# Performance work log

Hardware: AMD Instinct MI355X
Metric: run time of the kernel (lower is better)

The kernel has to match this reference:

```python
import jax, jax.numpy as jnp
import numpy as np

STATE_DIM = 32
ACTION_DIM = 8
IN_DIM = STATE_DIM + ACTION_DIM      # 40
DIMS = STATE_DIM + 1                 # 33 output dimensions (next-state deltas + reward)
ENS = 10                             # ensemble size
HID = 128
BATCH = 4096
MIN_LOGVAR = -10.0
MAX_LOGVAR = 5.0


def setup_inputs() -> dict:
    key = jax.random.key(0)
    ks = jax.random.split(key, 7)
    # Kaiming-uniform-ish init like torch Linear: U(-1/sqrt(fan_in), 1/sqrt(fan_in))
    def lin_init(k, shape, fan_in):
        bound = 1.0 / np.sqrt(fan_in)
        return jax.random.uniform(k, shape, jnp.float32, -bound, bound)
    x = jax.random.normal(ks[0], (BATCH, IN_DIM), jnp.float32)
    W1 = lin_init(ks[1], (DIMS, ENS, HID, IN_DIM), IN_DIM)
    b1 = lin_init(ks[2], (DIMS, ENS, HID), IN_DIM)
    W2 = lin_init(ks[3], (DIMS, ENS, HID, HID), HID)
    b2 = lin_init(ks[4], (DIMS, ENS, HID), HID)
    W3 = lin_init(ks[5], (DIMS, ENS, 2, HID), HID)
    b3 = lin_init(ks[6], (DIMS, ENS, 2), HID)
    return {"x": x, "W1": W1, "b1": b1, "W2": W2, "b2": b2, "W3": W3, "b3": b3}


def reference(x, W1, b1, W2, b2, W3, b3):
    # Batched over (d, e): all 330 small MLPs share the same input x.
    # h1: [B, D, E, H]
    h1 = jax.nn.silu(jnp.einsum('bi,dehi->bdeh', x, W1) + b1)
    h2 = jax.nn.silu(jnp.einsum('bdeh,degh->bdeg', h1, W2) + b2)
    out = jnp.einsum('bdeh,deoh->bdeo', h2, W3) + b3  # [B, D, E, 2]
    mean = out[..., 0]                                # [B, D, E]
    logvar = out[..., 1]
    # logvar soft clamp (same as original: two softplus bounds)
    logvar = MAX_LOGVAR - jax.nn.softplus(MAX_LOGVAR - logvar)
    logvar = MIN_LOGVAR + jax.nn.softplus(logvar - MIN_LOGVAR)
    # means[b, d, e] == means_all[d][e][b, 0] of the torch module
    return mean, logvar
```

## Files before the change

### kernel.cpp

```cpp
#include <hip/hip_runtime.h>

typedef _Float16 half8_t __attribute__((ext_vector_type(8)));
typedef float    f32x4_t __attribute__((ext_vector_type(4)));
typedef unsigned int uint4_t __attribute__((ext_vector_type(4)));

#define OUT_HALF 1351680
#define NDE 330

#define OFF_X16    0u
#define OFF_MEANT  524288u
#define OFF_LOGVT  5931008u
#define OFF_W1H    11337728u
#define OFF_W3H    16744448u
#define OFF_W2H    18096128u
#define WS_PACKED_BYTES 28909568u

__device__ __forceinline__ float fast_silu(float x) {
    float e = __builtin_amdgcn_exp2f(x * -1.44269504f);
    return x * __builtin_amdgcn_rcpf(1.0f + e);
}

__device__ __forceinline__ float fast_softplus(float x) {
    float e = __builtin_amdgcn_exp2f(x * 1.44269504f);
    return __builtin_amdgcn_logf(1.0f + e) * 0.69314718f;
}

__device__ __forceinline__ unsigned pk_silu(float a, float b) {
    return __builtin_bit_cast(unsigned,
        __builtin_amdgcn_cvt_pkrtz(fast_silu(a), fast_silu(b)));
}

__global__ __launch_bounds__(256) void prep_x_kernel(const float* __restrict__ x,
                                                     _Float16* __restrict__ x16) {
    int idx = blockIdx.x * 256 + threadIdx.x;
    if (idx >= 4096 * 64) return;
    int b = idx >> 6, cc = idx & 63;
    float v = (cc < 40) ? x[b * 40 + cc] : (cc == 40 ? 1.0f : 0.0f);
    x16[idx] = (_Float16)v;
}

__global__ __launch_bounds__(256) void prep_all_kernel(
    const float* __restrict__ x,
    const float* __restrict__ W1, const float* __restrict__ b1,
    const float* __restrict__ W2, const float* __restrict__ W3,
    _Float16* __restrict__ x16, _Float16* __restrict__ w1h,
    _Float16* __restrict__ w2h, _Float16* __restrict__ w3h)
{
    const int blk = blockIdx.x;
    const int tid = threadIdx.x;
    if (blk < 1024) {
        int idx = blk * 256 + tid;
        int b = idx >> 6, cc = idx & 63;
        float v = (cc < 40) ? x[b * 40 + cc] : (cc == 40 ? 1.0f : 0.0f);
        x16[idx] = (_Float16)v;
        return;
    }
    if (blk < 1024 + NDE) {
        const int de = blk - 1024;
        const float* W1g = W1 + (size_t)de * (128 * 40);
        const float* b1g = b1 + (size_t)de * 128;
        const float* W3g = W3 + (size_t)de * 256;
        for (int s = tid; s < 1024; s += 256) {
            int ht = s >> 7, rem = s & 127, kf = rem >> 6, lane = rem & 63;
            int c = lane & 15, q = lane >> 4, h = ht * 16 + c;
            union { _Float16 hh[8]; half8_t v; } u;
            if (kf == 0) {
                f32x4_t a  = *(const f32x4_t*)&W1g[h * 40 + q * 8];
                f32x4_t bb = *(const f32x4_t*)&W1g[h * 40 + q * 8 + 4];
                #pragma unroll
                for (int r = 0; r < 4; r++) { u.hh[r] = (_Float16)a[r]; u.hh[4 + r] = (_Float16)bb[r]; }
            } else {
                #pragma unroll
                for (int r = 0; r < 8; r++) u.hh[r] = (_Float16)0.0f;
                if (q == 0) {
                    f32x4_t a  = *(const f32x4_t*)&W1g[h * 40 + 32];
                    f32x4_t bb = *(const f32x4_t*)&W1g[h * 40 + 36];
                    #pragma unroll
                    for (int r = 0; r < 4; r++) { u.hh[r] = (_Float16)a[r]; u.hh[4 + r] = (_Float16)bb[r]; }
                } else if (q == 1) {
                    u.hh[0] = (_Float16)b1g[h];
                }
            }
            *(half8_t*)&w1h[(size_t)de * 8192 + (ht * 2 + kf) * 512 + lane * 8] = u.v;
        }
        if (tid < 256) {
            int kf = tid >> 6, lane = tid & 63, c = lane & 15, q = lane >> 4;
            union { _Float16 hh[8]; half8_t v; } u;
            #pragma unroll
            for (int r = 0; r < 8; r++) u.hh[r] = (_Float16)0.0f;
            if (c < 2) {
                #pragma unroll
                for (int r = 0; r < 4; r++) {
                    u.hh[r]     = (_Float16)W3g[c * 128 + kf * 32 + q * 4 + r];
                    u.hh[4 + r] = (_Float16)W3g[c * 128 + kf * 32 + 16 + q * 4 + r];
                }
            }
            *(half8_t*)&w3h[(size_t)de * 2048 + kf * 512 + lane * 8] = u.v;
        }
        return;
    }
    int f = (blk - 1024 - NDE) * 256 + tid;
    if (f >= NDE * 2048) return;
    int de = f >> 11, i = f & 2047;
    int g = i >> 4, kf = (i >> 2) & 3, qq = i & 3;
    const float* W2g = W2 + (size_t)de * 16384;
    f32x4_t a  = *(const f32x4_t*)&W2g[g * 128 + kf * 32 + qq * 4];
    f32x4_t bb = *(const f32x4_t*)&W2g[g * 128 + kf * 32 + 16 + qq * 4];
    union { _Float16 hh[8]; half8_t v; } u;
    #pragma unroll
    for (int r = 0; r < 4; r++) { u.hh[r] = (_Float16)a[r]; u.hh[4 + r] = (_Float16)bb[r]; }
    int off = (((g >> 4) * 4 + kf) * 64 + qq * 16 + (g & 15)) * 8;
    *(half8_t*)&w2h[(size_t)de * 16384 + off] = u.v;
}

template <bool PACKED>
__global__ __launch_bounds__(512, 4) void mlp_kernel(
    const _Float16* __restrict__ x16,
    const float* __restrict__ W1, const float* __restrict__ b1,
    const float* __restrict__ W2, const float* __restrict__ b2,
    const float* __restrict__ W3, const float* __restrict__ b3,
    const _Float16* __restrict__ w1h, const _Float16* __restrict__ w2h,
    const _Float16* __restrict__ w3h,
    float* __restrict__ mean_t, float* __restrict__ logvar_t)
{
    __shared__ _Float16 w1s[8192];
    __shared__ _Float16 w2s[16384];
    __shared__ _Float16 w3s[2048];
    __shared__ float    b2s[128];

    const int bid   = blockIdx.x;
    const int grp   = bid >> 6;
    const int xcd   = bid & 7;
    const int chunk = (bid >> 3) & 7;
    const int de    = grp * 8 + xcd;
    if (de >= NDE) return;

    const int tid  = threadIdx.x;
    const int wave = tid >> 6;
    const int lane = tid & 63;
    const int c    = lane & 15;
    const int q    = lane >> 4;

    if constexpr (PACKED) {
        const _Float16* W1g = w1h + (size_t)de * 8192;
        *(half8_t*)&w1s[tid * 8]         = *(const half8_t*)&W1g[tid * 8];
        *(half8_t*)&w1s[(tid + 512) * 8] = *(const half8_t*)&W1g[(tid + 512) * 8];
        const _Float16* W2g = w2h + (size_t)de * 16384;
        #pragma unroll
        for (int i0 = 0; i0 < 4; i0++) {
            int i = tid + i0 * 512;
            *(half8_t*)&w2s[i * 8] = *(const half8_t*)&W2g[i * 8];
        }
        if (tid < 256)
            *(half8_t*)&w3s[tid * 8] = *(const half8_t*)&w3h[(size_t)de * 2048 + tid * 8];
    } else {
        {
            const float* W1g = W1 + (size_t)de * (128 * 40);
            const float* b1g = b1 + (size_t)de * 128;
            for (int s = tid; s < 1024; s += 512) {
                int ht = s >> 7, rem = s & 127, kff = rem >> 6, ln = rem & 63;
                int cc = ln & 15, qq = ln >> 4, h = ht * 16 + cc;
                union { _Float16 hh[8]; half8_t v; } u;
                if (kff == 0) {
                    f32x4_t a  = *(const f32x4_t*)&W1g[h * 40 + qq * 8];
                    f32x4_t bb = *(const f32x4_t*)&W1g[h * 40 + qq * 8 + 4];
                    #pragma unroll
                    for (int r = 0; r < 4; r++) { u.hh[r] = (_Float16)a[r]; u.hh[4 + r] = (_Float16)bb[r]; }
                } else {
                    #pragma unroll
                    for (int r = 0; r < 8; r++) u.hh[r] = (_Float16)0.0f;
                    if (qq == 0) {
                        f32x4_t a  = *(const f32x4_t*)&W1g[h * 40 + 32];
                        f32x4_t bb = *(const f32x4_t*)&W1g[h * 40 + 36];
                        #pragma unroll
                        for (int r = 0; r < 4; r++) { u.hh[r] = (_Float16)a[r]; u.hh[4 + r] = (_Float16)bb[r]; }
                    } else if (qq == 1) {
                        u.hh[0] = (_Float16)b1g[h];
                    }
                }
                *(half8_t*)&w1s[(ht * 2 + kff) * 512 + ln * 8] = u.v;
            }
        }
        const float* W2g = W2 + (size_t)de * 16384;
        #pragma unroll
        for (int i0 = 0; i0 < 4; i0++) {
            int i = tid + i0 * 512;
            int F = i >> 6, l = i & 63;
            int mt = F >> 2, kf = F & 3, q2 = l >> 4, c2 = l & 15;
            int g = mt * 16 + c2;
            f32x4_t a  = *(const f32x4_t*)&W2g[g * 128 + kf * 32 + q2 * 4];
            f32x4_t bb = *(const f32x4_t*)&W2g[g * 128 + kf * 32 + 16 + q2 * 4];
            union { _Float16 hh[8]; half8_t v; } u;
            #pragma unroll
            for (int r = 0; r < 4; r++) { u.hh[r] = (_Float16)a[r]; u.hh[4 + r] = (_Float16)bb[r]; }
            *(half8_t*)&w2s[i * 8] = u.v;
        }
        if (tid < 256) {
            const float* W3g = W3 + (size_t)de * 256;
            int kf = tid >> 6, ln = tid & 63, c2 = ln & 15, q2 = ln >> 4;
            union { _Float16 hh[8]; half8_t v; } u;
            #pragma unroll
            for (int r = 0; r < 8; r++) u.hh[r] = (_Float16)0.0f;
            if (c2 < 2) {
                #pragma unroll
                for (int r = 0; r < 4; r++) {
                    u.hh[r]     = (_Float16)W3g[c2 * 128 + kf * 32 + q2 * 4 + r];
                    u.hh[4 + r] = (_Float16)W3g[c2 * 128 + kf * 32 + 16 + q2 * 4 + r];
                }
            }
            *(half8_t*)&w3s[kf * 512 + ln * 8] = u.v;
        }
    }
    if (tid < 128) b2s[tid] = b2[de * 128 + tid];
    __syncthreads();

    const float b3m = b3[de * 2 + 0];
    const float b3l = b3[de * 2 + 1];
    const f32x4_t zero4 = {0.f, 0.f, 0.f, 0.f};

    const _Float16* const w1base = w1s + lane * 8;
    const _Float16* const w2base = w2s + lane * 8;
    const _Float16* const w3base = w3s + lane * 8;
    const float*    const b2base = b2s + q * 4;

    const int r0 = chunk * 512 + wave * 16 + c;
    const _Float16* px = x16 + (size_t)r0 * 64 + q * 8;
    float* pm = mean_t   + (size_t)de * 4096 + r0;
    float* pl = logvar_t + (size_t)de * 4096 + r0;

    #pragma unroll 1
    for (int it = 0; it < 4; it++) {
        half8_t xf0 = *(const half8_t*)(px);
        half8_t xf1 = *(const half8_t*)(px + 32);

        f32x4_t acc2[8];
        #pragma unroll
        for (int mt = 0; mt < 8; mt++)
            acc2[mt] = *(const f32x4_t*)(b2base + mt * 16);

        const _Float16* pw1 = w1base;
        const _Float16* paf = w2base;
        #pragma unroll 1
        for (int kf = 0; kf < 4; kf++) {
            uint4_t bu;
            #pragma unroll
            for (int h2 = 0; h2 < 2; h2++) {
                half8_t a0 = *(const half8_t*)(pw1 + h2 * 1024);
                half8_t a1 = *(const half8_t*)(pw1 + h2 * 1024 + 512);
                f32x4_t a = __builtin_amdgcn_mfma_f32_16x16x32_f16(a0, xf0, zero4, 0, 0, 0);
                f32x4_t t = __builtin_amdgcn_mfma_f32_16x16x32_f16(a1, xf1, a, 0, 0, 0);
                bu[2 * h2 + 0] = pk_silu(t[0], t[1]);
                bu[2 * h2 + 1] = pk_silu(t[2], t[3]);
            }
            const half8_t bh = __builtin_bit_cast(half8_t, bu);
            #pragma unroll
            for (int mt = 0; mt < 8; mt++) {
                half8_t af = *(const half8_t*)(paf + mt * 2048);
                acc2[mt] = __builtin_amdgcn_mfma_f32_16x16x32_f16(af, bh, acc2[mt], 0, 0, 0);
            }
            pw1 += 2048;
            paf += 512;
        }

        f32x4_t acc3 = zero4;
        #pragma unroll
        for (int kf2 = 0; kf2 < 4; kf2++) {
            half8_t w3f = *(const half8_t*)(w3base + kf2 * 512);
            uint4_t bu;
            bu[0] = pk_silu(acc2[kf2 * 2 + 0][0], acc2[kf2 * 2 + 0][1]);
            bu[1] = pk_silu(acc2[kf2 * 2 + 0][2], acc2[kf2 * 2 + 0][3]);
            bu[2] = pk_silu(acc2[kf2 * 2 + 1][0], acc2[kf2 * 2 + 1][1]);
            bu[3] = pk_silu(acc2[kf2 * 2 + 1][2], acc2[kf2 * 2 + 1][3]);
            acc3 = __builtin_amdgcn_mfma_f32_16x16x32_f16(
                w3f, __builtin_bit_cast(half8_t, bu), acc3, 0, 0, 0);
        }

        if (q == 0) {
            float vm = acc3[0] + b3m;
            float vl = acc3[1] + b3l;
            vl = 5.0f - fast_softplus(5.0f - vl);
            vl = -10.0f + fast_softplus(vl + 10.0f);
            pm[0] = vm;
            pl[0] = vl;
        }
        px += 128 * 64;
        pm += 128;
        pl += 128;
    }
}

__global__ __launch_bounds__(256) void transpose_out_kernel(
    const float* __restrict__ mean_t, const float* __restrict__ logvar_t,
    float* __restrict__ out)
{
    __shared__ float tile[32][33];
    const int bg0 = blockIdx.x * 32;
    const int de0 = blockIdx.y * 32;
    const float* src = blockIdx.z ? logvar_t : mean_t;
    float* dst = blockIdx.z ? (out + OUT_HALF) : out;
    const int cidx = threadIdx.x & 31;
    const int r0   = threadIdx.x >> 5;
    #pragma unroll
    for (int k = 0; k < 4; k++) {
        int de_l = r0 + k * 8;
        if (de0 + de_l < NDE)
            tile[de_l][cidx] = src[(size_t)(de0 + de_l) * 4096 + bg0 + cidx];
    }
    __syncthreads();
    #pragma unroll
    for (int k = 0; k < 4; k++) {
        int bg_l = r0 + k * 8;
        if (de0 + cidx < NDE)
            dst[(size_t)(bg0 + bg_l) * 330 + de0 + cidx] = tile[cidx][bg_l];
    }
}

extern "C" void kernel_launch(void* const* d_in, const int* in_sizes, int n_in,
                              void* d_out, int out_size, void* d_ws, size_t ws_size,
                              hipStream_t stream) {
    (void)in_sizes; (void)n_in; (void)out_size;
    const float* x  = (const float*)d_in[0];
    const float* W1 = (const float*)d_in[1];
    const float* b1 = (const float*)d_in[2];
    const float* W2 = (const float*)d_in[3];
    const float* b2 = (const float*)d_in[4];
    const float* W3 = (const float*)d_in[5];
    const float* b3 = (const float*)d_in[6];
    float* out = (float*)d_out;

    char* ws = (char*)d_ws;
    _Float16* x16   = (_Float16*)(ws + OFF_X16);
    float* mean_t   = (float*)(ws + OFF_MEANT);
    float* logvar_t = (float*)(ws + OFF_LOGVT);

    const int MLP_GRID = 42 * 64;

    if (ws_size >= WS_PACKED_BYTES) {
        _Float16* w1h = (_Float16*)(ws + OFF_W1H);
        _Float16* w3h = (_Float16*)(ws + OFF_W3H);
        _Float16* w2h = (_Float16*)(ws + OFF_W2H);
        hipLaunchKernelGGL(prep_all_kernel, dim3(1024 + NDE + 2640), dim3(256), 0, stream,
                           x, W1, b1, W2, W3, x16, w1h, w2h, w3h);
        hipLaunchKernelGGL((mlp_kernel<true>), dim3(MLP_GRID), dim3(512), 0, stream,
                           x16, W1, b1, W2, b2, W3, b3, w1h, w2h, w3h, mean_t, logvar_t);
    } else {
        hipLaunchKernelGGL(prep_x_kernel, dim3(1024), dim3(256), 0, stream, x, x16);
        hipLaunchKernelGGL((mlp_kernel<false>), dim3(MLP_GRID), dim3(512), 0, stream,
                           x16, W1, b1, W2, b2, W3, b3, x16, x16, x16, mean_t, logvar_t);
    }
    hipLaunchKernelGGL(transpose_out_kernel, dim3(128, 11, 2), dim3(256), 0, stream,
                       mean_t, logvar_t, out);
}
```

Baseline: 198.2 us.

## Stream W2 fragments from global, halve block size, fold log2e/ln2 into weights

The packed path no longer stages W2 in shared memory. Each wave now reads its W2 MFMA fragments directly from global/L2 through a relaid-out packed buffer, and blocks shrink to 256 threads with 5 blocks per CU and 8 row iterations each. SiLU's exp scaling is folded into W1, b1 and b2 by premultiplying with log2(e), and its output scaling is folded into W3 with ln2, so each activation drops a multiply. The intent is to cut LDS usage and raise occupancy. The cost is repeated global loads of W2 inside the inner loop and some extra fp16 rounding from the prescaled weights.

Result: slower. 301.2 us (+52.0%).

```diff
diff --git a/kernel.cpp b/kernel.cpp
--- a/kernel.cpp
+++ b/kernel.cpp
@@ -15,19 +15,20 @@
 #define OFF_W2H    18096128u
 #define WS_PACKED_BYTES 28909568u
 
-__device__ __forceinline__ float fast_silu(float x) {
-    float e = __builtin_amdgcn_exp2f(x * -1.44269504f);
-    return x * __builtin_amdgcn_rcpf(1.0f + e);
-}
+#define C_LOG2E 1.44269504088896f
+#define C_LN2   0.69314718055995f
 
 __device__ __forceinline__ float fast_softplus(float x) {
     float e = __builtin_amdgcn_exp2f(x * 1.44269504f);
     return __builtin_amdgcn_logf(1.0f + e) * 0.69314718f;
 }
 
-__device__ __forceinline__ unsigned pk_silu(float a, float b) {
-    return __builtin_bit_cast(unsigned,
-        __builtin_amdgcn_cvt_pkrtz(fast_silu(a), fast_silu(b)));
+__device__ __forceinline__ unsigned pk_g(float u0, float u1) {
+    float e0 = __builtin_amdgcn_exp2f(-u0);
+    float e1 = __builtin_amdgcn_exp2f(-u1);
+    float g0 = u0 * __builtin_amdgcn_rcpf(1.0f + e0);
+    float g1 = u1 * __builtin_amdgcn_rcpf(1.0f + e1);
+    return __builtin_bit_cast(unsigned, __builtin_amdgcn_cvt_pkrtz(g0, g1));
 }
 
 __global__ __launch_bounds__(256) void prep_x_kernel(const float* __restrict__ x,
@@ -68,7 +69,10 @@
                 f32x4_t a  = *(const f32x4_t*)&W1g[h * 40 + q * 8];
                 f32x4_t bb = *(const f32x4_t*)&W1g[h * 40 + q * 8 + 4];
                 #pragma unroll
-                for (int r = 0; r < 4; r++) { u.hh[r] = (_Float16)a[r]; u.hh[4 + r] = (_Float16)bb[r]; }
+                for (int r = 0; r < 4; r++) {
+                    u.hh[r]     = (_Float16)(a[r]  * C_LOG2E);
+                    u.hh[4 + r] = (_Float16)(bb[r] * C_LOG2E);
+                }
             } else {
                 #pragma unroll
                 for (int r = 0; r < 8; r++) u.hh[r] = (_Float16)0.0f;
@@ -76,9 +80,12 @@
                     f32x4_t a  = *(const f32x4_t*)&W1g[h * 40 + 32];
                     f32x4_t bb = *(const f32x4_t*)&W1g[h * 40 + 36];
                     #pragma unroll
-                    for (int r = 0; r < 4; r++) { u.hh[r] = (_Float16)a[r]; u.hh[4 + r] = (_Float16)bb[r]; }
+                    for (int r = 0; r < 4; r++) {
+                        u.hh[r]     = (_Float16)(a[r]  * C_LOG2E);
+                        u.hh[4 + r] = (_Float16)(bb[r] * C_LOG2E);
+                    }
                 } else if (q == 1) {
-                    u.hh[0] = (_Float16)b1g[h];
+                    u.hh[0] = (_Float16)(b1g[h] * C_LOG2E);
                 }
             }
             *(half8_t*)&w1h[(size_t)de * 8192 + (ht * 2 + kf) * 512 + lane * 8] = u.v;
@@ -91,8 +98,8 @@
             if (c < 2) {
                 #pragma unroll
                 for (int r = 0; r < 4; r++) {
-                    u.hh[r]     = (_Float16)W3g[c * 128 + kf * 32 + q * 4 + r];
-                    u.hh[4 + r] = (_Float16)W3g[c * 128 + kf * 32 + 16 + q * 4 + r];
+                    u.hh[r]     = (_Float16)(W3g[c * 128 + kf * 32 + q * 4 + r]      * C_LN2);
+                    u.hh[4 + r] = (_Float16)(W3g[c * 128 + kf * 32 + 16 + q * 4 + r] * C_LN2);
                 }
             }
             *(half8_t*)&w3h[(size_t)de * 2048 + kf * 512 + lane * 8] = u.v;
@@ -109,12 +116,13 @@
     union { _Float16 hh[8]; half8_t v; } u;
     #pragma unroll
     for (int r = 0; r < 4; r++) { u.hh[r] = (_Float16)a[r]; u.hh[4 + r] = (_Float16)bb[r]; }
-    int off = (((g >> 4) * 4 + kf) * 64 + qq * 16 + (g & 15)) * 8;
+    int mt = g >> 4, c2 = g & 15;
+    int off = ((kf * 8 + mt) * 64 + qq * 16 + c2) * 8;
     *(half8_t*)&w2h[(size_t)de * 16384 + off] = u.v;
 }
 
 template <bool PACKED>
-__global__ __launch_bounds__(512, 4) void mlp_kernel(
+__global__ __launch_bounds__(256, 5) void mlp_kernel(
     const _Float16* __restrict__ x16,
     const float* __restrict__ W1, const float* __restrict__ b1,
     const float* __restrict__ W2, const float* __restrict__ b2,
@@ -124,9 +132,9 @@
     float* __restrict__ mean_t, float* __restrict__ logvar_t)
 {
     __shared__ _Float16 w1s[8192];
-    __shared__ _Float16 w2s[16384];
     __shared__ _Float16 w3s[2048];
     __shared__ float    b2s[128];
+    __shared__ _Float16 w2s_fb[PACKED ? 8 : 16384];
 
     const int bid   = blockIdx.x;
     const int grp   = bid >> 6;
@@ -143,21 +151,17 @@
 
     if constexpr (PACKED) {
         const _Float16* W1g = w1h + (size_t)de * 8192;
-        *(half8_t*)&w1s[tid * 8]         = *(const half8_t*)&W1g[tid * 8];
-        *(half8_t*)&w1s[(tid + 512) * 8] = *(const half8_t*)&W1g[(tid + 512) * 8];
-        const _Float16* W2g = w2h + (size_t)de * 16384;
         #pragma unroll
         for (int i0 = 0; i0 < 4; i0++) {
-            int i = tid + i0 * 512;
-            *(half8_t*)&w2s[i * 8] = *(const half8_t*)&W2g[i * 8];
-        }
-        if (tid < 256)
-            *(half8_t*)&w3s[tid * 8] = *(const half8_t*)&w3h[(size_t)de * 2048 + tid * 8];
+            int i = tid + i0 * 256;
+            *(half8_t*)&w1s[i * 8] = *(const half8_t*)&W1g[i * 8];
+        }
+        *(half8_t*)&w3s[tid * 8] = *(const half8_t*)&w3h[(size_t)de * 2048 + tid * 8];
     } else {
         {
             const float* W1g = W1 + (size_t)de * (128 * 40);
             const float* b1g = b1 + (size_t)de * 128;
-            for (int s = tid; s < 1024; s += 512) {
+            for (int s = tid; s < 1024; s += 256) {
                 int ht = s >> 7, rem = s & 127, kff = rem >> 6, ln = rem & 63;
                 int cc = ln & 15, qq = ln >> 4, h = ht * 16 + cc;
                 union { _Float16 hh[8]; half8_t v; } u;
@@ -165,7 +169,10 @@
                     f32x4_t a  = *(const f32x4_t*)&W1g[h * 40 + qq * 8];
                     f32x4_t bb = *(const f32x4_t*)&W1g[h * 40 + qq * 8 + 4];
                     #pragma unroll
-                    for (int r = 0; r < 4; r++) { u.hh[r] = (_Float16)a[r]; u.hh[4 + r] = (_Float16)bb[r]; }
+                    for (int r = 0; r < 4; r++) {
+                        u.hh[r]     = (_Float16)(a[r]  * C_LOG2E);
+                        u.hh[4 + r] = (_Float16)(bb[r] * C_LOG2E);
+                    }
                 } else {
                     #pragma unroll
                     for (int r = 0; r < 8; r++) u.hh[r] = (_Float16)0.0f;
@@ -173,9 +180,12 @@
                         f32x4_t a  = *(const f32x4_t*)&W1g[h * 40 + 32];
                         f32x4_t bb = *(const f32x4_t*)&W1g[h * 40 + 36];
                         #pragma unroll
-                        for (int r = 0; r < 4; r++) { u.hh[r] = (_Float16)a[r]; u.hh[4 + r] = (_Float16)bb[r]; }
+                        for (int r = 0; r < 4; r++) {
+                            u.hh[r]     = (_Float16)(a[r]  * C_LOG2E);
+                            u.hh[4 + r] = (_Float16)(bb[r] * C_LOG2E);
+                        }
                     } else if (qq == 1) {
-                        u.hh[0] = (_Float16)b1g[h];
+                        u.hh[0] = (_Float16)(b1g[h] * C_LOG2E);
                     }
                 }
                 *(half8_t*)&w1s[(ht * 2 + kff) * 512 + ln * 8] = u.v;
@@ -183,8 +193,8 @@
         }
         const float* W2g = W2 + (size_t)de * 16384;
         #pragma unroll
-        for (int i0 = 0; i0 < 4; i0++) {
-            int i = tid + i0 * 512;
+        for (int i0 = 0; i0 < 8; i0++) {
+            int i = tid + i0 * 256;
             int F = i >> 6, l = i & 63;
             int mt = F >> 2, kf = F & 3, q2 = l >> 4, c2 = l & 15;
             int g = mt * 16 + c2;
@@ -193,9 +203,9 @@
             union { _Float16 hh[8]; half8_t v; } u;
             #pragma unroll
             for (int r = 0; r < 4; r++) { u.hh[r] = (_Float16)a[r]; u.hh[4 + r] = (_Float16)bb[r]; }
-            *(half8_t*)&w2s[i * 8] = u.v;
-        }
-        if (tid < 256) {
+            *(half8_t*)&w2s_fb[i * 8] = u.v;
+        }
+        {
             const float* W3g = W3 + (size_t)de * 256;
             int kf = tid >> 6, ln = tid & 63, c2 = ln & 15, q2 = ln >> 4;
             union { _Float16 hh[8]; half8_t v; } u;
@@ -204,14 +214,14 @@
             if (c2 < 2) {
                 #pragma unroll
                 for (int r = 0; r < 4; r++) {
-                    u.hh[r]     = (_Float16)W3g[c2 * 128 + kf * 32 + q2 * 4 + r];
-                    u.hh[4 + r] = (_Float16)W3g[c2 * 128 + kf * 32 + 16 + q2 * 4 + r];
+                    u.hh[r]     = (_Float16)(W3g[c2 * 128 + kf * 32 + q2 * 4 + r]      * C_LN2);
+                    u.hh[4 + r] = (_Float16)(W3g[c2 * 128 + kf * 32 + 16 + q2 * 4 + r] * C_LN2);
                 }
             }
             *(half8_t*)&w3s[kf * 512 + ln * 8] = u.v;
         }
     }
-    if (tid < 128) b2s[tid] = b2[de * 128 + tid];
+    if (tid < 128) b2s[tid] = b2[de * 128 + tid] * C_LOG2E;
     __syncthreads();
 
     const float b3m = b3[de * 2 + 0];
@@ -219,9 +229,11 @@
     const f32x4_t zero4 = {0.f, 0.f, 0.f, 0.f};
 
     const _Float16* const w1base = w1s + lane * 8;
-    const _Float16* const w2base = w2s + lane * 8;
     const _Float16* const w3base = w3s + lane * 8;
     const float*    const b2base = b2s + q * 4;
+    const _Float16* const pf2A = w2h + (size_t)de * 16384 + lane * 8;
+    const _Float16* const pf2B = pf2A + 2048;
+    const _Float16* const paf_fb = w2s_fb + lane * 8;
 
     const int r0 = chunk * 512 + wave * 16 + c;
     const _Float16* px = x16 + (size_t)r0 * 64 + q * 8;
@@ -229,7 +241,7 @@
     float* pl = logvar_t + (size_t)de * 4096 + r0;
 
     #pragma unroll 1
-    for (int it = 0; it < 4; it++) {
+    for (int it = 0; it < 8; it++) {
         half8_t xf0 = *(const half8_t*)(px);
         half8_t xf1 = *(const half8_t*)(px + 32);
 
@@ -239,7 +251,9 @@
             acc2[mt] = *(const f32x4_t*)(b2base + mt * 16);
 
         const _Float16* pw1 = w1base;
-        const _Float16* paf = w2base;
+        const _Float16* pfA = pf2A;
+        const _Float16* pfB = pf2B;
+        const _Float16* paf = paf_fb;
         #pragma unroll 1
         for (int kf = 0; kf < 4; kf++) {
             uint4_t bu;
@@ -249,16 +263,24 @@
                 half8_t a1 = *(const half8_t*)(pw1 + h2 * 1024 + 512);
                 f32x4_t a = __builtin_amdgcn_mfma_f32_16x16x32_f16(a0, xf0, zero4, 0, 0, 0);
                 f32x4_t t = __builtin_amdgcn_mfma_f32_16x16x32_f16(a1, xf1, a, 0, 0, 0);
-                bu[2 * h2 + 0] = pk_silu(t[0], t[1]);
-                bu[2 * h2 + 1] = pk_silu(t[2], t[3]);
+                bu[2 * h2 + 0] = pk_g(t[0], t[1]);
+                bu[2 * h2 + 1] = pk_g(t[2], t[3]);
             }
             const half8_t bh = __builtin_bit_cast(half8_t, bu);
             #pragma unroll
             for (int mt = 0; mt < 8; mt++) {
-                half8_t af = *(const half8_t*)(paf + mt * 2048);
+                half8_t af;
+                if constexpr (PACKED) {
+                    af = (mt < 4) ? *(const half8_t*)(pfA + mt * 512)
+                                  : *(const half8_t*)(pfB + (mt - 4) * 512);
+                } else {
+                    af = *(const half8_t*)(paf + mt * 2048);
+                }
                 acc2[mt] = __builtin_amdgcn_mfma_f32_16x16x32_f16(af, bh, acc2[mt], 0, 0, 0);
             }
             pw1 += 2048;
+            pfA += 4096;
+            pfB += 4096;
             paf += 512;
         }
 
@@ -267,10 +289,10 @@
         for (int kf2 = 0; kf2 < 4; kf2++) {
             half8_t w3f = *(const half8_t*)(w3base + kf2 * 512);
             uint4_t bu;
-            bu[0] = pk_silu(acc2[kf2 * 2 + 0][0], acc2[kf2 * 2 + 0][1]);
-            bu[1] = pk_silu(acc2[kf2 * 2 + 0][2], acc2[kf2 * 2 + 0][3]);
-            bu[2] = pk_silu(acc2[kf2 * 2 + 1][0], acc2[kf2 * 2 + 1][1]);
-            bu[3] = pk_silu(acc2[kf2 * 2 + 1][2], acc2[kf2 * 2 + 1][3]);
+            bu[0] = pk_g(acc2[kf2 * 2 + 0][0], acc2[kf2 * 2 + 0][1]);
+            bu[1] = pk_g(acc2[kf2 * 2 + 0][2], acc2[kf2 * 2 + 0][3]);
+            bu[2] = pk_g(acc2[kf2 * 2 + 1][0], acc2[kf2 * 2 + 1][1]);
+            bu[3] = pk_g(acc2[kf2 * 2 + 1][2], acc2[kf2 * 2 + 1][3]);
             acc3 = __builtin_amdgcn_mfma_f32_16x16x32_f16(
                 w3f, __builtin_bit_cast(half8_t, bu), acc3, 0, 0, 0);
         }
@@ -283,9 +305,9 @@
             pm[0] = vm;
             pl[0] = vl;
         }
-        px += 128 * 64;
-        pm += 128;
-        pl += 128;
+        px += 64 * 64;
+        pm += 64;
+        pl += 64;
     }
 }
 
@@ -341,11 +363,11 @@
         _Float16* w2h = (_Float16*)(ws + OFF_W2H);
         hipLaunchKernelGGL(prep_all_kernel, dim3(1024 + NDE + 2640), dim3(256), 0, stream,
                            x, W1, b1, W2, W3, x16, w1h, w2h, w3h);
-        hipLaunchKernelGGL((mlp_kernel<true>), dim3(MLP_GRID), dim3(512), 0, stream,
+        hipLaunchKernelGGL((mlp_kernel<true>), dim3(MLP_GRID), dim3(256), 0, stream,
                            x16, W1, b1, W2, b2, W3, b3, w1h, w2h, w3h, mean_t, logvar_t);
     } else {
         hipLaunchKernelGGL(prep_x_kernel, dim3(1024), dim3(256), 0, stream, x, x16);
-        hipLaunchKernelGGL((mlp_kernel<false>), dim3(MLP_GRID), dim3(512), 0, stream,
+        hipLaunchKernelGGL((mlp_kernel<false>), dim3(MLP_GRID), dim3(256), 0, stream,
                            x16, W1, b1, W2, b2, W3, b3, x16, x16, x16, mean_t, logvar_t);
     }
     hipLaunchKernelGGL(transpose_out_kernel, dim3(128, 11, 2), dim3(256), 0, stream,
```
